# Kernel tuning notes

Hardware: AMD Instinct MI355X
Metric: run time of the kernel (lower is better)

The kernel has to match this reference:

```python
import jax, jax.numpy as jnp
import numpy as np

EPS = 1e-6

def _feature_map(x):
    # elu_feature_map: elu(x) + 1
    return jax.nn.elu(x) + 1.0

def setup_inputs() -> dict:
    key = jax.random.key(0)
    ks = jax.random.split(key, 7)
    B, C, H, W = 4, 128, 32, 32
    s = 1.0 / np.sqrt(C)
    return {
        "feature": jax.random.normal(ks[0], (B, C, H, W), dtype=jnp.float32),
        "wq": jax.random.normal(ks[1], (C, C), dtype=jnp.float32) * s,
        "bq": jax.random.normal(ks[2], (C,), dtype=jnp.float32) * s,
        "wk": jax.random.normal(ks[3], (C, C), dtype=jnp.float32) * s,
        "bk": jax.random.normal(ks[4], (C,), dtype=jnp.float32) * s,
        "wv": jax.random.normal(ks[5], (C, C), dtype=jnp.float32) * s,
        "bv": jax.random.normal(ks[6], (C,), dtype=jnp.float32) * s,
    }

def reference(feature, wq, bq, wk, bk, wv, bv):
    B, C, H, W = feature.shape
    # flatten(2).transpose(1,2): (B, C, H*W) -> (B, N, C)
    x = feature.reshape(B, C, H * W).transpose(0, 2, 1)
    # torch Linear: x @ W.T + b
    query = x @ wq.T + bq
    key_p = x @ wk.T + bk
    value = x @ wv.T + bv
    Q = _feature_map(query)  # (B, N, C)
    K = _feature_map(key_p)  # (B, N, C)
    # state=None path: Si = 0 + K; Ri = 0 + outer(K, V)
    Si = K                                           # (B, N, C)
    Ri = jnp.einsum('bnc,bnm->bncm', K, value)       # (B, N, C, M)
    Z = 1.0 / (jnp.einsum('bnc,bnc->bn', Q, Si) + EPS)  # (B, N)
    RLSA = jnp.einsum('bnc,bncm,bn->bnm', Q, Ri, Z)  # (B, N, M)
    return (RLSA, Ri, Si)
```

## Files before the change

### kernel.cpp

```cpp
#include <hip/hip_runtime.h>
#include <math.h>

#define C 128
#define N 1024
#define EPS 1e-6f

typedef float f32x4 __attribute__((ext_vector_type(4)));

#define TR 8
#define XS_STRIDE 12

__global__ __launch_bounds__(256) void fused_kernel(
    const float* __restrict__ feat,
    const float* __restrict__ wq, const float* __restrict__ bq,
    const float* __restrict__ wk, const float* __restrict__ bk,
    const float* __restrict__ wv, const float* __restrict__ bv,
    float* __restrict__ out_rlsa, float* __restrict__ out_ri,
    float* __restrict__ out_si)
{
    __shared__ float xs[C * XS_STRIDE];
    __shared__ float sred[4][4];
    __shared__ float ks[TR * C];
    __shared__ float vs[TR * C];

    const int t    = threadIdx.x;
    const int c    = t & 127;
    const int half = t >> 7;
    const int row0 = blockIdx.x * TR;
    const int b    = row0 >> 10;
    const int n0   = row0 & 1023;

    {
        const float* fb = feat + (size_t)b * C * N;
        int j = t >> 1, q = t & 1;
        float4 v = *(const float4*)(fb + (size_t)j * N + n0 + q * 4);
        *(float4*)&xs[j * XS_STRIDE + q * 4] = v;
    }
    __syncthreads();

    float aq[4] = {0}, ak[4] = {0}, av[4] = {0};
    const float4* wq4 = (const float4*)(wq + c * C);
    const float4* wk4 = (const float4*)(wk + c * C);
    const float4* wv4 = (const float4*)(wv + c * C);
    const int xoff = half * 4;

    #pragma unroll 8
    for (int j4 = 0; j4 < 32; ++j4) {
        float4 q4 = wq4[j4];
        float4 k4 = wk4[j4];
        float4 v4 = wv4[j4];
        #pragma unroll
        for (int u = 0; u < 4; ++u) {
            float4 xa = *(const float4*)&xs[(j4 * 4 + u) * XS_STRIDE + xoff];
            float wqv = (u == 0) ? q4.x : (u == 1) ? q4.y : (u == 2) ? q4.z : q4.w;
            float wkv = (u == 0) ? k4.x : (u == 1) ? k4.y : (u == 2) ? k4.z : k4.w;
            float wvv = (u == 0) ? v4.x : (u == 1) ? v4.y : (u == 2) ? v4.z : v4.w;
            aq[0] += xa.x * wqv; aq[1] += xa.y * wqv; aq[2] += xa.z * wqv; aq[3] += xa.w * wqv;
            ak[0] += xa.x * wkv; ak[1] += xa.y * wkv; ak[2] += xa.z * wkv; ak[3] += xa.w * wkv;
            av[0] += xa.x * wvv; av[1] += xa.y * wvv; av[2] += xa.z * wvv; av[3] += xa.w * wvv;
        }
    }

    const float bqc = bq[c], bkc = bk[c], bvc = bv[c];
    float qf[4], kf[4], vf[4];
    #pragma unroll
    for (int i = 0; i < 4; ++i) {
        float q = aq[i] + bqc;
        float k = ak[i] + bkc;
        qf[i] = q > 0.f ? q + 1.f : expf(q);
        kf[i] = k > 0.f ? k + 1.f : expf(k);
        vf[i] = av[i] + bvc;
    }

    const int wave = t >> 6;
    const int lane = t & 63;
    #pragma unroll
    for (int i = 0; i < 4; ++i) {
        float p = qf[i] * kf[i];
        #pragma unroll
        for (int off = 32; off > 0; off >>= 1) p += __shfl_down(p, off, 64);
        if (lane == 0) sred[wave][i] = p;
    }
    __syncthreads();

    #pragma unroll
    for (int i = 0; i < 4; ++i) {
        float S = sred[half * 2][i] + sred[half * 2 + 1][i];
        float coef = S / (S + EPS);
        int r = half * 4 + i;
        size_t ro = (size_t)(row0 + r) * C + c;
        out_si[ro]   = kf[i];
        out_rlsa[ro] = coef * vf[i];
        ks[r * C + c] = kf[i];
        vs[r * C + c] = vf[i];
    }
    __syncthreads();

    const f32x4* vs4 = (const f32x4*)vs;
    #pragma unroll
    for (int r = 0; r < TR; ++r) {
        f32x4* ri4 = (f32x4*)(out_ri + (size_t)(row0 + r) * C * C);
        const float* krow  = ks  + r * C;
        const f32x4* vrow4 = vs4 + r * 32;
        #pragma unroll
        for (int i = 0; i < 16; ++i) {
            int f4 = i * 256 + t;
            float kc = krow[f4 >> 5];
            f32x4 vv = vrow4[f4 & 31];
            f32x4 o  = kc * vv;
            __builtin_nontemporal_store(o, ri4 + f4);
        }
    }
}

extern "C" void kernel_launch(void* const* d_in, const int* in_sizes, int n_in,
                              void* d_out, int out_size, void* d_ws, size_t ws_size,
                              hipStream_t stream) {
    const float* feat = (const float*)d_in[0];
    const float* wq   = (const float*)d_in[1];
    const float* bq   = (const float*)d_in[2];
    const float* wk   = (const float*)d_in[3];
    const float* bk   = (const float*)d_in[4];
    const float* wv   = (const float*)d_in[5];
    const float* bv   = (const float*)d_in[6];

    float* out  = (float*)d_out;
    float* rlsa = out;
    float* ri   = out + (size_t)4 * 1024 * 128;
    float* si   = ri  + (size_t)4 * 1024 * 128 * 128;

    fused_kernel<<<4096 / TR, 256, 0, stream>>>(feat, wq, bq, wk, bk, wv, bv,
                                                rlsa, ri, si);
}
```

Before: 308.7 us.

## Split fused kernel into QKV projection and separate Ri outer-product kernel

Splits the single fused kernel in two. The first computes Q/K/V, RLSA and Si and writes V to workspace. The second reads K and V back and writes the 256 MB Ri outer-product output with more, smaller blocks, regular stores instead of nontemporal ones, and V held in registers per thread. This separates the compute-heavy projection from the bandwidth-bound store phase so each can reach better occupancy, at the cost of an extra launch and a small round-trip of K/V through global memory.

```diff
diff --git a/kernel.cpp b/kernel.cpp
--- a/kernel.cpp
+++ b/kernel.cpp
@@ -10,18 +10,16 @@
 #define TR 8
 #define XS_STRIDE 12
 
-__global__ __launch_bounds__(256) void fused_kernel(
+__global__ __launch_bounds__(256) void qkv_kernel(
     const float* __restrict__ feat,
     const float* __restrict__ wq, const float* __restrict__ bq,
     const float* __restrict__ wk, const float* __restrict__ bk,
     const float* __restrict__ wv, const float* __restrict__ bv,
-    float* __restrict__ out_rlsa, float* __restrict__ out_ri,
-    float* __restrict__ out_si)
+    float* __restrict__ out_rlsa, float* __restrict__ out_si,
+    float* __restrict__ ws_v)
 {
     __shared__ float xs[C * XS_STRIDE];
     __shared__ float sred[4][4];
-    __shared__ float ks[TR * C];
-    __shared__ float vs[TR * C];
 
     const int t    = threadIdx.x;
     const int c    = t & 127;
@@ -44,7 +42,7 @@
     const float4* wv4 = (const float4*)(wv + c * C);
     const int xoff = half * 4;
 
-    #pragma unroll 8
+    #pragma unroll 4
     for (int j4 = 0; j4 < 32; ++j4) {
         float4 q4 = wq4[j4];
         float4 k4 = wk4[j4];
@@ -87,28 +85,47 @@
     for (int i = 0; i < 4; ++i) {
         float S = sred[half * 2][i] + sred[half * 2 + 1][i];
         float coef = S / (S + EPS);
-        int r = half * 4 + i;
-        size_t ro = (size_t)(row0 + r) * C + c;
+        size_t ro = (size_t)(row0 + half * 4 + i) * C + c;
         out_si[ro]   = kf[i];
         out_rlsa[ro] = coef * vf[i];
-        ks[r * C + c] = kf[i];
-        vs[r * C + c] = vf[i];
+        ws_v[ro]     = vf[i];
+    }
+}
+
+#define BROWS 4
+
+__global__ __launch_bounds__(256) void ri_kernel(
+    const float* __restrict__ si, const float* __restrict__ ws_v,
+    float* __restrict__ out_ri)
+{
+    __shared__ float ks[BROWS * C];
+    __shared__ float vs[BROWS * C];
+
+    const int t  = threadIdx.x;
+    const int r0 = blockIdx.x * BROWS;
+
+    {
+        const f32x4* si4 = (const f32x4*)(si   + (size_t)r0 * C);
+        const f32x4* wv4 = (const f32x4*)(ws_v + (size_t)r0 * C);
+        f32x4* ks4 = (f32x4*)ks;
+        f32x4* vs4 = (f32x4*)vs;
+        if (t < 128) ks4[t] = si4[t];
+        else         vs4[t - 128] = wv4[t - 128];
     }
     __syncthreads();
 
-    const f32x4* vs4 = (const f32x4*)vs;
+    const int t5 = t >> 5;
+    const int tm = t & 31;
+
     #pragma unroll
-    for (int r = 0; r < TR; ++r) {
-        f32x4* ri4 = (f32x4*)(out_ri + (size_t)(row0 + r) * C * C);
-        const float* krow  = ks  + r * C;
-        const f32x4* vrow4 = vs4 + r * 32;
+    for (int r = 0; r < BROWS; ++r) {
+        f32x4* ri4 = (f32x4*)(out_ri + (size_t)(r0 + r) * C * C);
+        const float* krow = ks + r * C;
+        f32x4 vv = ((const f32x4*)(vs + r * C))[tm];
         #pragma unroll
         for (int i = 0; i < 16; ++i) {
-            int f4 = i * 256 + t;
-            float kc = krow[f4 >> 5];
-            f32x4 vv = vrow4[f4 & 31];
-            f32x4 o  = kc * vv;
-            __builtin_nontemporal_store(o, ri4 + f4);
+            float kc = krow[i * 8 + t5];
+            ri4[i * 256 + t] = kc * vv;
         }
     }
 }
@@ -129,6 +146,9 @@
     float* ri   = out + (size_t)4 * 1024 * 128;
     float* si   = ri  + (size_t)4 * 1024 * 128 * 128;
 
-    fused_kernel<<<4096 / TR, 256, 0, stream>>>(feat, wq, bq, wk, bk, wv, bv,
-                                                rlsa, ri, si);
+    float* ws_v = (float*)d_ws;
+
+    qkv_kernel<<<4096 / TR, 256, 0, stream>>>(feat, wq, bq, wk, bk, wv, bv,
+                                              rlsa, si, ws_v);
+    ri_kernel<<<4096 / BROWS, 256, 0, stream>>>(si, ws_v, ri);
 }
```

Result: no change. 306.8 us (-0.6%).
